# Kernel optimization log

Hardware: AMD Instinct MI355X
Metric: run time of the kernel (lower is better)

## Reference

```python
import jax, jax.numpy as jnp
import numpy as np

H = 32  # hidden_size
I = 1   # input_size
O = 1   # output_size


def setup_inputs() -> dict:
    key = jax.random.key(0)
    ks = jax.random.split(key, 7)
    T, B = 2048, 2048
    s_ih = 1.0 / np.sqrt(H)
    return {
        "x": jax.random.normal(ks[0], (T, B, I), dtype=jnp.float32),
        "W_ih": jax.random.uniform(ks[1], (4 * H, I), jnp.float32, -s_ih, s_ih),
        "W_hh": jax.random.uniform(ks[2], (4 * H, H), jnp.float32, -s_ih, s_ih),
        "b_ih": jax.random.uniform(ks[3], (4 * H,), jnp.float32, -s_ih, s_ih),
        "b_hh": jax.random.uniform(ks[4], (4 * H,), jnp.float32, -s_ih, s_ih),
        "W_out": jax.random.uniform(ks[5], (O, H), jnp.float32, -s_ih, s_ih),
        "b_out": jax.random.uniform(ks[6], (O,), jnp.float32, -s_ih, s_ih),
    }


def _lstm(x, W_ih, W_hh, b_ih, b_hh):
    T, B, _ = x.shape
    # Precompute input contribution for all timesteps: [T, B, 4H]
    x_gates = jnp.einsum('tbi,gi->tbg', x, W_ih) + b_ih + b_hh

    def step(carry, xg):
        h, c = carry
        gates = xg + h @ W_hh.T  # [B, 4H]
        i, f, g, o = jnp.split(gates, 4, axis=-1)  # PyTorch gate order i,f,g,o
        i = jax.nn.sigmoid(i)
        f = jax.nn.sigmoid(f)
        g = jnp.tanh(g)
        o = jax.nn.sigmoid(o)
        c = f * c + i * g
        h = o * jnp.tanh(c)
        return (h, c), h

    h0 = jnp.zeros((B, H), dtype=x.dtype)
    c0 = jnp.zeros((B, H), dtype=x.dtype)
    (hT, cT), r_out = jax.lax.scan(step, (h0, c0), x_gates)
    return r_out, (hT[None], cT[None])  # match PyTorch [num_layers, B, H] state


def reference(x, W_ih, W_hh, b_ih, b_hh, W_out, b_out):
    r_out, state = _lstm(x, W_ih, W_hh, b_ih, b_hh)  # [T, B, H]
    outs = jnp.einsum('tbh,oh->tbo', r_out, W_out) + b_out  # [T, B, O]
    return outs, state
```

## Files before the change

kernel.cpp:

```cpp
#include <hip/hip_runtime.h>


namespace {
constexpr int T_ = 2048;
constexpr int B_ = 2048;
constexpr int H_ = 32;
constexpr int WPB = 4;
constexpr int EPB = WPB * 2;
constexpr int CHUNK = 32;
constexpr int NCH = T_ / CHUNK;
constexpr int OUTS = T_ * B_;
constexpr float L2E = 1.442695040888963f;

typedef float v2f __attribute__((ext_vector_type(2)));
typedef float v4f __attribute__((ext_vector_type(4)));

__device__ __forceinline__ float rcp_(float v){ return __builtin_amdgcn_rcpf(v); }
__device__ __forceinline__ float ex2_(float v){ return __builtin_amdgcn_exp2f(v); }

template <int CTRL, int RM, int BM, bool BC>
__device__ __forceinline__ float dpp_add(float acc, float src) {
    int mv = __builtin_amdgcn_update_dpp(0, __builtin_bit_cast(int, src),
                                         CTRL, RM, BM, BC);
    return acc + __builtin_bit_cast(float, mv);
}
__device__ __forceinline__ float half_sum32(float v) {
    v = dpp_add<0x111, 0xF, 0xF, true >(v, v);
    v = dpp_add<0x112, 0xF, 0xF, true >(v, v);
    v = dpp_add<0x114, 0xF, 0xF, true >(v, v);
    v = dpp_add<0x118, 0xF, 0xF, true >(v, v);
    v = dpp_add<0x142, 0xA, 0xF, false>(v, v);
    return v;
}
}

__global__ __launch_bounds__(256, 1)
__attribute__((amdgpu_num_vgpr(256)))
void lstm_fused10(
    const float* __restrict__ x,
    const float* __restrict__ W_ih,
    const float* __restrict__ W_hh,
    const float* __restrict__ b_ih,
    const float* __restrict__ b_hh,
    const float* __restrict__ W_out,
    const float* __restrict__ b_out,
    float* __restrict__ out)
{
    const int l  = threadIdx.x & 63;
    const int wv = threadIdx.x >> 6;
    const int j  = l & 31;
    const int p  = l >> 5;
    const int e  = blockIdx.x * EPB + wv * 2 + p;

    __shared__ __align__(16) float hbuf[WPB][2][H_];

    const float sI = -L2E, sF = -L2E, sG = 2.0f * L2E, sO = -L2E;

    v2f wi[H_/2], wf[H_/2], wg[H_/2], wo[H_/2];
#pragma unroll
    for (int k2 = 0; k2 < H_/2; ++k2) {
        const float* ri = W_hh + (0*H_ + j) * H_;
        const float* rf = W_hh + (1*H_ + j) * H_;
        const float* rg = W_hh + (2*H_ + j) * H_;
        const float* ro = W_hh + (3*H_ + j) * H_;
        wi[k2] = (v2f){ ri[2*k2] * sI, ri[2*k2+1] * sI };
        wf[k2] = (v2f){ rf[2*k2] * sF, rf[2*k2+1] * sF };
        wg[k2] = (v2f){ rg[2*k2] * sG, rg[2*k2+1] * sG };
        wo[k2] = (v2f){ ro[2*k2] * sO, ro[2*k2+1] * sO };
    }
#pragma unroll
    for (int k2 = 0; k2 < H_/2; ++k2) {
        __asm__ __volatile__("" : "+v"(wi[k2]));
        __asm__ __volatile__("" : "+v"(wf[k2]));
        __asm__ __volatile__("" : "+v"(wg[k2]));
        __asm__ __volatile__("" : "+v"(wo[k2]));
    }

    const float wxi = W_ih[0*H_+j] * sI, wxf = W_ih[1*H_+j] * sF;
    const float wxg = W_ih[2*H_+j] * sG, wxo = W_ih[3*H_+j] * sO;
    const float bi  = (b_ih[0*H_+j] + b_hh[0*H_+j]) * sI;
    const float bf  = (b_ih[1*H_+j] + b_hh[1*H_+j]) * sF;
    const float bg  = (b_ih[2*H_+j] + b_hh[2*H_+j]) * sG;
    const float bo_ = (b_ih[3*H_+j] + b_hh[3*H_+j]) * sO;
    const float wout = W_out[j];
    const float bout = b_out[0];

    float c = 0.0f, h = 0.0f;
    hbuf[wv][p][j] = 0.0f;
    __asm__ __volatile__("" ::: "memory");
    v4f hq[H_/4];
#pragma unroll
    for (int q = 0; q < H_/4; ++q)
        hq[q] = ((const v4f*)&hbuf[wv][p][0])[q];

    float xcur = x[j * B_ + e];
    int outOff = e;

    for (int ch = 0; ch < NCH; ++ch) {
        float xnext = 0.0f;
        if (ch + 1 < NCH) xnext = x[((ch + 1) * CHUNK + j) * B_ + e];
#pragma unroll 8
        for (int s = 0; s < CHUNK; ++s) {
            const int xr0 = __builtin_amdgcn_readlane(__builtin_bit_cast(int, xcur), s);
            const int xr1 = __builtin_amdgcn_readlane(__builtin_bit_cast(int, xcur), s + 32);
            const float xk = p ? __builtin_bit_cast(float, xr1)
                               : __builtin_bit_cast(float, xr0);
            v2f ai0 = {bi  + xk * wxi, 0.f}, ai1 = {0.f, 0.f};
            v2f af0 = {bf  + xk * wxf, 0.f}, af1 = {0.f, 0.f};
            v2f ag0 = {bg  + xk * wxg, 0.f}, ag1 = {0.f, 0.f};
            v2f ao0 = {bo_ + xk * wxo, 0.f}, ao1 = {0.f, 0.f};
#pragma unroll
            for (int q = 0; q < H_/4; ++q) {
                const v2f hlo = (v2f){ hq[q].x, hq[q].y };
                const v2f hhi = (v2f){ hq[q].z, hq[q].w };
                ai0 += wi[2*q] * hlo;  ai1 += wi[2*q+1] * hhi;
                af0 += wf[2*q] * hlo;  af1 += wf[2*q+1] * hhi;
                ag0 += wg[2*q] * hlo;  ag1 += wg[2*q+1] * hhi;
                ao0 += wo[2*q] * hlo;  ao1 += wo[2*q+1] * hhi;
            }
            const v2f ai = ai0 + ai1, af = af0 + af1;
            const v2f ag = ag0 + ag1, ao = ao0 + ao1;
            const float iv = rcp_(1.0f + ex2_(ai.x + ai.y));
            const float fv = rcp_(1.0f + ex2_(af.x + af.y));
            const float gv = 1.0f - 2.0f * rcp_(1.0f + ex2_(ag.x + ag.y));
            const float ov = rcp_(1.0f + ex2_(ao.x + ao.y));
            c = fv * c + iv * gv;
            const float tc = 1.0f - 2.0f * rcp_(1.0f + ex2_((2.0f * L2E) * c));
            h = ov * tc;
            hbuf[wv][p][j] = h;
            __asm__ __volatile__("" ::: "memory");
#pragma unroll
            for (int q = 0; q < H_/4; ++q)
                hq[q] = ((const v4f*)&hbuf[wv][p][0])[q];
            const float pr = half_sum32(h * wout);
            if ((l & 31) == 31) out[outOff] = pr + bout;
            outOff += B_;
        }
        xcur = xnext;
    }
    out[OUTS + e * H_ + j] = h;
    out[OUTS + B_ * H_ + e * H_ + j] = c;
}

extern "C" void kernel_launch(void* const* d_in, const int* in_sizes, int n_in,
                              void* d_out, int out_size, void* d_ws, size_t ws_size,
                              hipStream_t stream) {
    const float* x     = (const float*)d_in[0];
    const float* W_ih  = (const float*)d_in[1];
    const float* W_hh  = (const float*)d_in[2];
    const float* b_ih  = (const float*)d_in[3];
    const float* b_hh  = (const float*)d_in[4];
    const float* W_out = (const float*)d_in[5];
    const float* b_out = (const float*)d_in[6];
    lstm_fused10<<<dim3(B_ / EPB), dim3(256), 0, stream>>>(
        x, W_ih, W_hh, b_ih, b_hh, W_out, b_out, (float*)d_out);
}
```

Baseline: 715.6 us.

## Split each hidden unit's gates across lane pairs, one batch element per wave

Each wave now handles one batch element instead of two. Two adjacent lanes share a hidden unit: the even lane computes the i and g gates, the odd lane computes f and o, and the i*g product is exchanged with a DPP pair swap. This halves the recurrent multiply-adds per lane on the serial per-step path and doubles the number of waves, with launch bounds raised to allow two blocks per CU for latency hiding. It costs a cross-lane swap per step, a 64-lane reduction for the output projection, and redundant c updates on the even lanes.

```diff
diff --git a/kernel.cpp b/kernel.cpp
--- a/kernel.cpp
+++ b/kernel.cpp
@@ -6,8 +6,8 @@
 constexpr int B_ = 2048;
 constexpr int H_ = 32;
 constexpr int WPB = 4;
-constexpr int EPB = WPB * 2;
-constexpr int CHUNK = 32;
+constexpr int EPB = WPB;
+constexpr int CHUNK = 64;
 constexpr int NCH = T_ / CHUNK;
 constexpr int OUTS = T_ * B_;
 constexpr float L2E = 1.442695040888963f;
@@ -24,19 +24,24 @@
                                          CTRL, RM, BM, BC);
     return acc + __builtin_bit_cast(float, mv);
 }
-__device__ __forceinline__ float half_sum32(float v) {
+__device__ __forceinline__ float wave_sum64(float v) {
     v = dpp_add<0x111, 0xF, 0xF, true >(v, v);
     v = dpp_add<0x112, 0xF, 0xF, true >(v, v);
     v = dpp_add<0x114, 0xF, 0xF, true >(v, v);
     v = dpp_add<0x118, 0xF, 0xF, true >(v, v);
     v = dpp_add<0x142, 0xA, 0xF, false>(v, v);
+    v = dpp_add<0x143, 0xC, 0xF, false>(v, v);
     return v;
+}
+__device__ __forceinline__ float pair_swap(float v) {
+    int mv = __builtin_amdgcn_update_dpp(0, __builtin_bit_cast(int, v),
+                                         0xB1, 0xF, 0xF, true);
+    return __builtin_bit_cast(float, mv);
 }
 }
 
-__global__ __launch_bounds__(256, 1)
-__attribute__((amdgpu_num_vgpr(256)))
-void lstm_fused10(
+__global__ __launch_bounds__(256, 2)
+void lstm_fused11(
     const float* __restrict__ x,
     const float* __restrict__ W_ih,
     const float* __restrict__ W_hh,
@@ -46,100 +51,100 @@
     const float* __restrict__ b_out,
     float* __restrict__ out)
 {
-    const int l  = threadIdx.x & 63;
-    const int wv = threadIdx.x >> 6;
-    const int j  = l & 31;
-    const int p  = l >> 5;
-    const int e  = blockIdx.x * EPB + wv * 2 + p;
+    const int l   = threadIdx.x & 63;
+    const int wv  = threadIdx.x >> 6;
+    const int j   = l >> 1;
+    const int odd = l & 1;
+    const int e   = blockIdx.x * EPB + wv;
 
-    __shared__ __align__(16) float hbuf[WPB][2][H_];
+    __shared__ __align__(16) float hbuf[WPB][2 * H_];
 
-    const float sI = -L2E, sF = -L2E, sG = 2.0f * L2E, sO = -L2E;
+    const float sclA = -L2E;
+    const float sclB = odd ? -L2E : 2.0f * L2E;
+    const int rowA = odd ? (1*H_ + j) : j;
+    const int rowB = odd ? (3*H_ + j) : (2*H_ + j);
 
-    v2f wi[H_/2], wf[H_/2], wg[H_/2], wo[H_/2];
+    v2f wA[H_/2], wB[H_/2];
 #pragma unroll
     for (int k2 = 0; k2 < H_/2; ++k2) {
-        const float* ri = W_hh + (0*H_ + j) * H_;
-        const float* rf = W_hh + (1*H_ + j) * H_;
-        const float* rg = W_hh + (2*H_ + j) * H_;
-        const float* ro = W_hh + (3*H_ + j) * H_;
-        wi[k2] = (v2f){ ri[2*k2] * sI, ri[2*k2+1] * sI };
-        wf[k2] = (v2f){ rf[2*k2] * sF, rf[2*k2+1] * sF };
-        wg[k2] = (v2f){ rg[2*k2] * sG, rg[2*k2+1] * sG };
-        wo[k2] = (v2f){ ro[2*k2] * sO, ro[2*k2+1] * sO };
+        const float* rA = W_hh + rowA * H_;
+        const float* rB = W_hh + rowB * H_;
+        wA[k2] = (v2f){ rA[2*k2] * sclA, rA[2*k2+1] * sclA };
+        wB[k2] = (v2f){ rB[2*k2] * sclB, rB[2*k2+1] * sclB };
     }
 #pragma unroll
     for (int k2 = 0; k2 < H_/2; ++k2) {
-        __asm__ __volatile__("" : "+v"(wi[k2]));
-        __asm__ __volatile__("" : "+v"(wf[k2]));
-        __asm__ __volatile__("" : "+v"(wg[k2]));
-        __asm__ __volatile__("" : "+v"(wo[k2]));
+        __asm__ __volatile__("" : "+v"(wA[k2]));
+        __asm__ __volatile__("" : "+v"(wB[k2]));
     }
 
-    const float wxi = W_ih[0*H_+j] * sI, wxf = W_ih[1*H_+j] * sF;
-    const float wxg = W_ih[2*H_+j] * sG, wxo = W_ih[3*H_+j] * sO;
-    const float bi  = (b_ih[0*H_+j] + b_hh[0*H_+j]) * sI;
-    const float bf  = (b_ih[1*H_+j] + b_hh[1*H_+j]) * sF;
-    const float bg  = (b_ih[2*H_+j] + b_hh[2*H_+j]) * sG;
-    const float bo_ = (b_ih[3*H_+j] + b_hh[3*H_+j]) * sO;
-    const float wout = W_out[j];
+    const float wxA = W_ih[rowA] * sclA;
+    const float wxB = W_ih[rowB] * sclB;
+    const float bA  = (b_ih[rowA] + b_hh[rowA]) * sclA;
+    const float bB  = (b_ih[rowB] + b_hh[rowB]) * sclB;
+    const float cB0 = odd ? 0.0f :  1.0f;
+    const float cBm = odd ? 1.0f : -2.0f;
+    const float wout = odd ? W_out[j] : 0.0f;
     const float bout = b_out[0];
+    const int   hslot = odd ? j : (H_ + j);
 
     float c = 0.0f, h = 0.0f;
-    hbuf[wv][p][j] = 0.0f;
-    __asm__ __volatile__("" ::: "memory");
     v4f hq[H_/4];
 #pragma unroll
-    for (int q = 0; q < H_/4; ++q)
-        hq[q] = ((const v4f*)&hbuf[wv][p][0])[q];
+    for (int q = 0; q < H_/4; ++q) hq[q] = (v4f){0.f, 0.f, 0.f, 0.f};
 
-    float xcur = x[j * B_ + e];
+    float xcur = x[l * B_ + e];
     int outOff = e;
 
     for (int ch = 0; ch < NCH; ++ch) {
         float xnext = 0.0f;
-        if (ch + 1 < NCH) xnext = x[((ch + 1) * CHUNK + j) * B_ + e];
+        if (ch + 1 < NCH) xnext = x[((ch + 1) * CHUNK + l) * B_ + e];
 #pragma unroll 8
         for (int s = 0; s < CHUNK; ++s) {
-            const int xr0 = __builtin_amdgcn_readlane(__builtin_bit_cast(int, xcur), s);
-            const int xr1 = __builtin_amdgcn_readlane(__builtin_bit_cast(int, xcur), s + 32);
-            const float xk = p ? __builtin_bit_cast(float, xr1)
-                               : __builtin_bit_cast(float, xr0);
-            v2f ai0 = {bi  + xk * wxi, 0.f}, ai1 = {0.f, 0.f};
-            v2f af0 = {bf  + xk * wxf, 0.f}, af1 = {0.f, 0.f};
-            v2f ag0 = {bg  + xk * wxg, 0.f}, ag1 = {0.f, 0.f};
-            v2f ao0 = {bo_ + xk * wxo, 0.f}, ao1 = {0.f, 0.f};
+            const int xr = __builtin_amdgcn_readlane(__builtin_bit_cast(int, xcur), s);
+            const float xk = __builtin_bit_cast(float, xr);
+            const float xbA = bA + xk * wxA;
+            const float xbB = bB + xk * wxB;
+            v2f aA0 = wA[0] * (v2f){hq[0].x, hq[0].y};
+            v2f aA1 = wA[1] * (v2f){hq[0].z, hq[0].w};
+            v2f aB0 = wB[0] * (v2f){hq[0].x, hq[0].y};
+            v2f aB1 = wB[1] * (v2f){hq[0].z, hq[0].w};
 #pragma unroll
-            for (int q = 0; q < H_/4; ++q) {
-                const v2f hlo = (v2f){ hq[q].x, hq[q].y };
-                const v2f hhi = (v2f){ hq[q].z, hq[q].w };
-                ai0 += wi[2*q] * hlo;  ai1 += wi[2*q+1] * hhi;
-                af0 += wf[2*q] * hlo;  af1 += wf[2*q+1] * hhi;
-                ag0 += wg[2*q] * hlo;  ag1 += wg[2*q+1] * hhi;
-                ao0 += wo[2*q] * hlo;  ao1 += wo[2*q+1] * hhi;
+            for (int q = 1; q < H_/4; ++q) {
+                const v2f hlo = (v2f){hq[q].x, hq[q].y};
+                const v2f hhi = (v2f){hq[q].z, hq[q].w};
+                aA0 += wA[2*q]   * hlo;
+                aA1 += wA[2*q+1] * hhi;
+                aB0 += wB[2*q]   * hlo;
+                aB1 += wB[2*q+1] * hhi;
             }
-            const v2f ai = ai0 + ai1, af = af0 + af1;
-            const v2f ag = ag0 + ag1, ao = ao0 + ao1;
-            const float iv = rcp_(1.0f + ex2_(ai.x + ai.y));
-            const float fv = rcp_(1.0f + ex2_(af.x + af.y));
-            const float gv = 1.0f - 2.0f * rcp_(1.0f + ex2_(ag.x + ag.y));
-            const float ov = rcp_(1.0f + ex2_(ao.x + ao.y));
-            c = fv * c + iv * gv;
+            const v2f aAv = aA0 + aA1;
+            const v2f aBv = aB0 + aB1;
+            const float sA = aAv.x + aAv.y + xbA;
+            const float sB = aBv.x + aBv.y + xbB;
+            const float actA = rcp_(1.0f + ex2_(sA));
+            const float rB   = rcp_(1.0f + ex2_(sB));
+            const float gB   = cB0 + cBm * rB;
+            const float m    = actA * gB;
+            const float mrecv = pair_swap(m);
+            c = actA * c + mrecv;
             const float tc = 1.0f - 2.0f * rcp_(1.0f + ex2_((2.0f * L2E) * c));
-            h = ov * tc;
-            hbuf[wv][p][j] = h;
+            h = gB * tc;
+            hbuf[wv][hslot] = h;
             __asm__ __volatile__("" ::: "memory");
 #pragma unroll
             for (int q = 0; q < H_/4; ++q)
-                hq[q] = ((const v4f*)&hbuf[wv][p][0])[q];
-            const float pr = half_sum32(h * wout);
-            if ((l & 31) == 31) out[outOff] = pr + bout;
+                hq[q] = ((const v4f*)&hbuf[wv][0])[q];
+            const float pr = wave_sum64(h * wout);
+            if (l == 63) out[outOff] = pr + bout;
             outOff += B_;
         }
         xcur = xnext;
     }
-    out[OUTS + e * H_ + j] = h;
-    out[OUTS + B_ * H_ + e * H_ + j] = c;
+    if (odd) {
+        out[OUTS + e * H_ + j] = h;
+        out[OUTS + B_ * H_ + e * H_ + j] = c;
+    }
 }
 
 extern "C" void kernel_launch(void* const* d_in, const int* in_sizes, int n_in,
@@ -152,6 +157,6 @@
     const float* b_hh  = (const float*)d_in[4];
     const float* W_out = (const float*)d_in[5];
     const float* b_out = (const float*)d_in[6];
-    lstm_fused10<<<dim3(B_ / EPB), dim3(256), 0, stream>>>(
+    lstm_fused11<<<dim3(B_ / EPB), dim3(256), 0, stream>>>(
         x, W_ih, W_hh, b_ih, b_hh, W_out, b_out, (float*)d_out);
 }
```

Measured after the change: 766.7 us. +7.1%, slower.
